# Kernel tuning notes

Measured on AMD Instinct MI355X. Metric: run time of the kernel, lower is better.

The kernel has to match this reference:

```python
import jax, jax.numpy as jnp
import numpy as np
import math

# ---- model dims (match init_kwargs) ----
D_MODEL = 1024
EXPAND = 2
HEADDIM = 64
D_STATE = 128
NGROUPS = 1
CHUNK = 64
A_FLOOR = 1e-4
D_INNER = EXPAND * D_MODEL            # 2048
NHEADS = D_INNER // HEADDIM           # 32
ROPE_DIM = D_STATE // 2               # rope_fraction=0.5 -> rotate half the state dims
NROPE = ROPE_DIM // 2                 # 32 rotation angles
D_IN_PROJ = D_INNER + 2 * D_STATE * NGROUPS + 3 * NHEADS + NROPE  # 2432
B, L = 2, 2048
EPS = 1e-5


def setup_inputs() -> dict:
    key = jax.random.key(0)
    ks = jax.random.split(key, 5)
    u = jax.random.normal(ks[0], (B, L, D_MODEL), dtype=jnp.float32)
    W_in = jax.random.normal(ks[1], (D_IN_PROJ, D_MODEL), dtype=jnp.float32) * 0.02
    W_out = jax.random.normal(ks[2], (D_MODEL, D_INNER), dtype=jnp.float32) * 0.02
    # dt_bias init as in the torch module
    dt_min, dt_max, dt_floor = 1e-3, 1e-1, 1e-4
    dt = jnp.exp(jax.random.uniform(ks[3], (NHEADS,)) * (math.log(dt_max) - math.log(dt_min)) + math.log(dt_min))
    dt = jnp.maximum(dt, dt_floor)
    dt_bias = dt + jnp.log(-jnp.expm1(-dt))
    B_bias = jnp.ones((NHEADS, D_STATE), dtype=jnp.float32)
    C_bias = jnp.ones((NHEADS, D_STATE), dtype=jnp.float32)
    Bnorm_w = jnp.ones((D_STATE,), dtype=jnp.float32)
    Cnorm_w = jnp.ones((D_STATE,), dtype=jnp.float32)
    D = jnp.ones((NHEADS,), dtype=jnp.float32)
    return {"u": u, "W_in": W_in, "dt_bias": dt_bias, "B_bias": B_bias, "C_bias": C_bias,
            "Bnorm_w": Bnorm_w, "Cnorm_w": Cnorm_w, "D": D, "W_out": W_out}


def _rmsnorm(v, w):
    return v * jax.lax.rsqrt(jnp.mean(v * v, axis=-1, keepdims=True) + EPS) * w


def _rope(v, cos, sin):
    # rotate first 2*NROPE dims of last axis (pairs (i, i+NROPE)); rest untouched
    x1 = v[..., :NROPE]
    x2 = v[..., NROPE:2 * NROPE]
    rest = v[..., 2 * NROPE:]
    return jnp.concatenate([x1 * cos - x2 * sin, x1 * sin + x2 * cos, rest], axis=-1)


def _forward(u, W_in, dt_bias, B_bias, C_bias, Bnorm_w, Cnorm_w, D, W_out):
    b, l, _ = u.shape
    proj = jnp.einsum('bld,ed->ble', u, W_in)
    idx = np.cumsum([D_INNER, D_STATE * NGROUPS, D_STATE * NGROUPS, NHEADS, NHEADS, NHEADS])[:-1].tolist()
    x, Braw, Craw, dd_dt, dd_A, trap_angles = jnp.split(proj, [D_INNER, D_INNER + D_STATE, D_INNER + 2 * D_STATE,
                                                                D_INNER + 2 * D_STATE + NHEADS,
                                                                D_INNER + 2 * D_STATE + 2 * NHEADS], axis=-1)
    trap = trap_angles[..., :NHEADS]
    angles = trap_angles[..., NHEADS:NHEADS + NROPE]
    x = x.reshape(b, l, NHEADS, HEADDIM)

    # discretization scalars per (b,l,h)
    A = -jax.nn.softplus(dd_A)
    A = jnp.minimum(A, -A_FLOOR)
    DT = jax.nn.softplus(dd_dt + dt_bias)
    la = A * DT                      # log of per-step decay (negative)
    a = jnp.exp(la)

    # RMSNorm on B/C (ngroups=1), broadcast to heads, add per-head bias
    Bn = _rmsnorm(Braw, Bnorm_w)[:, :, None, :] + B_bias   # (b,l,h,n)
    Cn = _rmsnorm(Craw, Cnorm_w)[:, :, None, :] + C_bias

    # inline RoPE: cumulative angle Theta_t = cumsum(angles_t * dt_t)
    theta = angles[:, :, None, :] * DT[..., None]           # (b,l,h,r)
    Theta = jnp.cumsum(theta, axis=1)
    cosT, sinT = jnp.cos(Theta), jnp.sin(Theta)
    Bn = _rope(Bn, cosT, sinT)
    Cn = _rope(Cn, cosT, sinT)

    # trapezoidal integration weights: dt*(lam*B_t x_t + (1-lam)*exp(A dt)*B_{t-1} x_{t-1})
    lam = jax.nn.sigmoid(trap)
    w1 = DT * lam                    # current-token weight  (b,l,h)
    w2 = DT * (1.0 - lam) * a        # previous-token weight (includes decay)
    Bp = jnp.pad(Bn, ((0, 0), (1, 0), (0, 0), (0, 0)))[:, :-1]
    xp = jnp.pad(x, ((0, 0), (1, 0), (0, 0), (0, 0)))[:, :-1]

    # ---- chunked selective scan ----
    nc = l // CHUNK
    ck = lambda t: t.reshape(b, nc, CHUNK, *t.shape[2:])
    xc, xpc, Bc, Bpc, Cc = ck(x), ck(xp), ck(Bn), ck(Bp), ck(Cn)
    lac, w1c, w2c = ck(la), ck(w1), ck(w2)
    Acum = jnp.cumsum(lac, axis=2)                           # (b,z,t,h)

    mask = jnp.tril(jnp.ones((CHUNK, CHUNK), dtype=u.dtype))
    decay = jnp.exp(Acum[:, :, :, None, :] - Acum[:, :, None, :, :]) * mask[None, None, :, :, None]  # (b,z,t,s,h)

    CB1 = jnp.einsum('bzthn,bzshn->bztsh', Cc, Bc)
    CB2 = jnp.einsum('bzthn,bzshn->bztsh', Cc, Bpc)
    M1 = decay * CB1 * w1c[:, :, None, :, :]
    M2 = decay * CB2 * w2c[:, :, None, :, :]
    Yintra = jnp.einsum('bztsh,bzshp->bzthp', M1, xc) + jnp.einsum('bztsh,bzshp->bzthp', M2, xpc)

    # contribution of each chunk to its end-of-chunk state
    r = jnp.exp(Acum[:, :, -1:, :] - Acum)                   # (b,z,t,h)
    U = (jnp.einsum('bzsh,bzshn,bzshp->bzhpn', r * w1c, Bc, xc)
         + jnp.einsum('bzsh,bzshn,bzshp->bzhpn', r * w2c, Bpc, xpc))
    cd = jnp.exp(Acum[:, :, -1, :])                          # whole-chunk decay (b,z,h)

    def step(h, inp):
        U_, c_ = inp
        return c_[..., None, None] * h + U_, h               # emit state at chunk start
    h0 = jnp.zeros((b, NHEADS, HEADDIM, D_STATE), dtype=u.dtype)
    _, states = jax.lax.scan(step, h0, (jnp.moveaxis(U, 1, 0), jnp.moveaxis(cd, 1, 0)))  # (z,b,h,p,n)

    Ystate = jnp.einsum('bzthn,bzth,zbhpn->bzthp', Cc, jnp.exp(Acum), states)
    y = (Yintra + Ystate).reshape(b, l, NHEADS, HEADDIM) + x * D[None, None, :, None]
    y = y.reshape(b, l, D_INNER)
    return jnp.einsum('bli,oi->blo', y, W_out)


def reference(u, W_in, dt_bias, B_bias, C_bias, Bnorm_w, Cnorm_w, D, W_out):
    return _forward(u, W_in, dt_bias, B_bias, C_bias, Bnorm_w, Cnorm_w, D, W_out)
```

## Files before the change

kernel.cpp:

```cpp
#include <hip/hip_runtime.h>
#include <hip/hip_bf16.h>
#include <math.h>

typedef unsigned short u16;
typedef __attribute__((ext_vector_type(8))) short s16x8;
typedef __attribute__((ext_vector_type(4))) float f32x4;

#define BB 2
#define LL 2048
#define DMODEL 1024
#define DI 2048
#define NH 32
#define HD 64
#define DS 128
#define NR 32
#define CH 64
#define NC 32
#define DIP 2432
#define NTOK (BB*LL)
#define PAW 384
#define CVW 264

__device__ __forceinline__ float bf2f(u16 u){ union{unsigned i; float f;} c; c.i=((unsigned)u)<<16; return c.f; }
__device__ __forceinline__ u16 f2bf(float f){ __hip_bfloat16 h=__float2bfloat16(f); return *reinterpret_cast<u16*>(&h); }
__device__ __forceinline__ float softplusf(float x){ return fmaxf(x,0.f) + log1pf(expf(-fabsf(x))); }

__device__ __forceinline__ void gl_lds16(const void* g, void* l){
  __builtin_amdgcn_global_load_lds((const __attribute__((address_space(1))) void*)g,
                                   (__attribute__((address_space(3))) void*)l, 16, 0, 0);
}

__device__ __forceinline__ s16x8 ldswz(const u16* base, int r, int kunit){
  return *(const s16x8*)&base[r*128 + ((kunit ^ (r&7))<<3)];
}
__device__ __forceinline__ s16x8 ldswz64(const u16* base, int r, int kunit){
  return *(const s16x8*)&base[r*64 + ((kunit ^ (r&7))<<3)];
}
__device__ __forceinline__ float ldswz64_s(const u16* base, int r, int n){
  return bf2f(base[r*64 + (((n>>3) ^ (r&7))<<3) + (n&7)]);
}
__device__ __forceinline__ s16x8 ld72(const u16* base, int r, int kelem){
  return *(const s16x8*)&base[r*72 + kelem];
}

__global__ __launch_bounds__(256) void k_cast(const float* __restrict__ in, u16* __restrict__ out, int n){
  int i = (blockIdx.x*256 + threadIdx.x)*4;
  if (i < n){
    float4 v = *(const float4*)&in[i];
    ushort4 o; o.x=f2bf(v.x); o.y=f2bf(v.y); o.z=f2bf(v.z); o.w=f2bf(v.w);
    *(ushort4*)&out[i] = o;
  }
}

__global__ __launch_bounds__(512) void k_gemm_in(const u16* __restrict__ A,
                                                 const u16* __restrict__ Bm,
                                                 float* __restrict__ pAux,
                                                 u16* __restrict__ Xtg){
  __shared__ u16 lA[128*64];
  __shared__ u16 lB[128*64];
  int tid = threadIdx.x;
  int l = tid & 63, w = tid >> 6;
  int nwg = gridDim.x*gridDim.y;
  int flat = blockIdx.y*gridDim.x + blockIdx.x;
  int cpx = nwg >> 3;
  int swz = (flat & 7)*cpx + (flat >> 3);
  int bx = swz % gridDim.x, by = swz / gridDim.x;
  int bm = by*128, bn = bx*128;
  int wr = w >> 2, wc = w & 3;
  const f32x4 vzero = {0.f,0.f,0.f,0.f};
  f32x4 acc[4][2];
  #pragma unroll
  for (int i=0;i<4;i++)
    #pragma unroll
    for (int j=0;j<2;j++) acc[i][j] = vzero;

  for (int kt=0; kt<DMODEL; kt+=64){
    __syncthreads();
    #pragma unroll
    for (int cc=0; cc<2; cc++){
      int s = w*2 + cc;
      int uu = s*64 + l;
      int r = uu >> 3, jl = uu & 7;
      int j = jl ^ (r & 7);
      gl_lds16(A  + (size_t)(bm+r)*DMODEL + kt + j*8, &lA[s*512]);
      gl_lds16(Bm + (size_t)(bn+r)*DMODEL + kt + j*8, &lB[s*512]);
    }
    __syncthreads();
    #pragma unroll
    for (int ks=0; ks<2; ks++){
      s16x8 af[4], bf[2];
      #pragma unroll
      for (int i=0;i<4;i++){
        int row = wr*64 + i*16 + (l&15);
        int j = ks*4 + (l>>4);
        af[i] = *(const s16x8*)&lA[row*64 + (j^(row&7))*8];
      }
      #pragma unroll
      for (int i=0;i<2;i++){
        int row = wc*32 + i*16 + (l&15);
        int j = ks*4 + (l>>4);
        bf[i] = *(const s16x8*)&lB[row*64 + (j^(row&7))*8];
      }
      #pragma unroll
      for (int i=0;i<4;i++)
        #pragma unroll
        for (int jj=0;jj<2;jj++)
          acc[i][jj] = __builtin_amdgcn_mfma_f32_16x16x32_bf16(af[i], bf[jj], acc[i][jj], 0,0,0);
    }
  }
  int col0 = bn + wc*32 + (l&15);
  int row0 = bm + wr*64 + (l>>4)*4;
  if (bn < DI){
    int h = (bn + wc*32) >> 6;
    int pbase = (wc & 1)*32 + (l&15);
    int b = bm >> 11;
    #pragma unroll
    for (int i=0;i<4;i++){
      int lbase = (bm & (LL-1)) + wr*64 + (l>>4)*4 + i*16;
      #pragma unroll
      for (int jj=0;jj<2;jj++){
        int p = pbase + jj*16;
        ushort4 o;
        o.x = f2bf(acc[i][jj][0]); o.y = f2bf(acc[i][jj][1]);
        o.z = f2bf(acc[i][jj][2]); o.w = f2bf(acc[i][jj][3]);
        *(ushort4*)&Xtg[((size_t)(b*NH + h)*HD + p)*LL + lbase] = o;
      }
    }
  } else {
    #pragma unroll
    for (int i=0;i<4;i++)
      #pragma unroll
      for (int jj=0;jj<2;jj++)
        #pragma unroll
        for (int q=0;q<4;q++)
          pAux[(size_t)(row0 + i*16 + q)*PAW + col0 + jj*16 - DI] = acc[i][jj][q];
  }
}

__global__ __launch_bounds__(256) void k_prep(const float* __restrict__ pAux,
                                              const float* __restrict__ dt_bias,
                                              const float* __restrict__ Bnw,
                                              const float* __restrict__ Cnw,
                                              float* __restrict__ Bnr, float* __restrict__ Cnr,
                                              float* __restrict__ DTg, float* __restrict__ lag,
                                              float* __restrict__ w1g, float* __restrict__ w2g){
  int tid = threadIdx.x;
  int r = tid >> 7, t = tid & 127;
  int row = blockIdx.x*2 + r;
  const float* pr = pAux + (size_t)row*PAW;
  float bv = pr[t], cv = pr[128+t];
  float sb = bv*bv, sc = cv*cv;
  for (int o=32;o;o>>=1){ sb += __shfl_down(sb,o); sc += __shfl_down(sc,o); }
  __shared__ float red[8];
  if ((tid&63)==0){ red[(tid>>6)*2]=sb; red[(tid>>6)*2+1]=sc; }
  __syncthreads();
  float ssb = red[r*4]+red[r*4+2], ssc = red[r*4+1]+red[r*4+3];
  float rb = rsqrtf(ssb/DS + 1e-5f), rc = rsqrtf(ssc/DS + 1e-5f);
  Bnr[(size_t)row*DS+t] = bv*rb*Bnw[t];
  Cnr[(size_t)row*DS+t] = cv*rc*Cnw[t];
  if (t < NH){
    int h = t;
    float Av = -softplusf(pr[288+h]); Av = fminf(Av, -1e-4f);
    float DT = softplusf(pr[256+h] + dt_bias[h]);
    float la = Av*DT;
    float lam = 1.f/(1.f+expf(-pr[320+h]));
    DTg[row*NH+h] = DT;
    lag[row*NH+h] = la;
    w1g[row*NH+h] = DT*lam;
    w2g[row*NH+h] = DT*(1.f-lam)*expf(la);
  }
}

__global__ __launch_bounds__(64) void k_theta_part(const float* __restrict__ pAux, const float* __restrict__ DTg,
                                                   float* __restrict__ Spart){
  int blk = blockIdx.x*2 + (threadIdx.x>>5);
  int j = threadIdx.x & 31;
  int h = blk % NH; int z = (blk/NH)%NC; int b = blk/(NH*NC);
  float acc = 0.f;
  for (int i=0;i<CH;i++){
    int row = b*LL + z*CH + i;
    acc += DTg[row*NH+h] * pAux[(size_t)row*PAW + 352 + j];
  }
  Spart[(size_t)blk*NR + j] = acc;
}

__global__ void k_theta_scan(float* __restrict__ Spart){
  int idx = blockIdx.x*blockDim.x + threadIdx.x;
  int j = idx % NR; int h = (idx/NR)%NH; int b = idx/(NR*NH);
  float acc = 0.f;
  for (int z=0;z<NC;z++){
    size_t o = (size_t)((b*NC+z)*NH + h)*NR + j;
    float t = Spart[o]; Spart[o] = acc; acc += t;
  }
}

__global__ __launch_bounds__(64) void k_theta_full(const float* __restrict__ pAux, const float* __restrict__ DTg,
                                                   const float* __restrict__ Spart, float* __restrict__ Theta){
  int blk = blockIdx.x*2 + (threadIdx.x>>5);
  int j = threadIdx.x & 31;
  int h = blk % NH; int z = (blk/NH)%NC; int b = blk/(NH*NC);
  float acc = Spart[(size_t)blk*NR + j];
  for (int i=0;i<CH;i++){
    int row = b*LL + z*CH + i;
    acc += DTg[row*NH+h] * pAux[(size_t)row*PAW + 352 + j];
    Theta[((size_t)row*NH + h)*NR + j] = acc;
  }
}

__global__ __launch_bounds__(256) void k_acum(const float* __restrict__ lag,
                                              const float* __restrict__ w1g,
                                              const float* __restrict__ w2g,
                                              float* __restrict__ CV,
                                              float* __restrict__ Acumg,
                                              float* __restrict__ cdg){
  int blk = blockIdx.x*4 + (threadIdx.x>>6);
  int l = threadIdx.x & 63;
  int h = blk & 31, z = (blk>>5)&31, b = blk>>10;
  int row = b*LL + z*CH + l;
  float la = lag[row*NH+h], w1 = w1g[row*NH+h], w2 = w2g[row*NH+h];
  float a = la;
  #pragma unroll
  for (int o=1;o<64;o<<=1){ float t = __shfl_up(a,o); a += (l>=o) ? t : 0.f; }
  float Acm = __shfl(a, 31);
  float Alast = __shfl(a, 63);
  float eA = expf(a - Acm);
  float emA = expf(Acm - a);
  float rfac = expf(Alast - a);
  float rw1 = rfac*w1, rw2 = rfac*w2;
  float rw1p = __shfl_up(rw1, 1);
  float* cv = CV + (size_t)blk*CVW;
  cv[l] = eA;
  cv[64 + l] = emA*w1;
  cv[128 + l] = emA*w2;
  cv[192 + l] = (l>0 ? rw1p : 0.f) + rw2;
  if (l == 63){ cv[192+64] = rw1; cdg[blk] = expf(Alast); }
  Acumg[(size_t)blk*CH + l] = a;
}

__global__ __launch_bounds__(256) void k_rope2(const float* __restrict__ Bnr,
                                               const float* __restrict__ Cnr,
                                               const float* __restrict__ Theta,
                                               const float* __restrict__ B_bias,
                                               const float* __restrict__ C_bias,
                                               const float* __restrict__ CV,
                                               u16* __restrict__ Bn, u16* __restrict__ Cn,
                                               u16* __restrict__ BTw){
  __shared__ float vwS[65];
  __shared__ u16 BTt[128][68];
  int blk = blockIdx.x; int h = blk&31, z=(blk>>5)&31, b=blk>>10;
  int l0 = z*CH; int tid = threadIdx.x;
  if (tid < 65) vwS[tid] = CV[(size_t)blk*CVW + 192 + tid];
  __syncthreads();
  #pragma unroll
  for (int it=0; it<8; it++){
    int idx = it*256 + tid;
    int r = idx>>5, j = idx&31;
    int row = b*LL + l0 + r;
    const float* br = Bnr + (size_t)row*DS;
    const float* cr = Cnr + (size_t)row*DS;
    const float* bb = B_bias + h*DS;
    const float* cb = C_bias + h*DS;
    float th = Theta[((size_t)row*NH + h)*NR + j];
    float cs = cosf(th), sn = sinf(th);
    float b0 = br[j]    + bb[j];
    float b1 = br[j+32] + bb[j+32];
    float b2 = br[j+64] + bb[j+64];
    float b3 = br[j+96] + bb[j+96];
    float c0 = cr[j]    + cb[j];
    float c1 = cr[j+32] + cb[j+32];
    float c2 = cr[j+64] + cb[j+64];
    float c3 = cr[j+96] + cb[j+96];
    float obA = b0*cs - b1*sn, obB = b0*sn + b1*cs;
    float ocA = c0*cs - c1*sn, ocB = c0*sn + c1*cs;
    u16* bnp = Bn + ((size_t)row*NH + h)*DS;
    u16* cnp = Cn + ((size_t)row*NH + h)*DS;
    bnp[j]    = f2bf(obA); bnp[j+32] = f2bf(obB);
    bnp[j+64] = f2bf(b2);  bnp[j+96] = f2bf(b3);
    cnp[j]    = f2bf(ocA); cnp[j+32] = f2bf(ocB);
    cnp[j+64] = f2bf(c2);  cnp[j+96] = f2bf(c3);
    float vwr = vwS[r+1];
    BTt[j][r]    = f2bf(obA*vwr);
    BTt[j+32][r] = f2bf(obB*vwr);
    BTt[j+64][r] = f2bf(b2*vwr);
    BTt[j+96][r] = f2bf(b3*vwr);
  }
  __syncthreads();
  for (int it=0; it<8; it++){
    int idx = it*256 + tid;
    int n = idx>>4, rg = (idx&15)*4;
    ushort4 o4;
    o4.x = BTt[n][rg];
    o4.y = BTt[n][rg+1];
    o4.z = BTt[n][rg+2];
    o4.w = BTt[n][rg+3];
    *(ushort4*)&BTw[((size_t)((b*NH+h)*DS) + n)*LL + l0 + rg] = o4;
  }
}

__global__ __launch_bounds__(256) void k_chunk_a(
    const u16* __restrict__ Xtg, const u16* __restrict__ Bn,
    const u16* __restrict__ Cn, const u16* __restrict__ BTw,
    const float* __restrict__ CV, const float* __restrict__ Dgl,
    u16* __restrict__ Yb, u16* __restrict__ Ugb){
  __shared__ u16 BsBT[65*128];
  __shared__ u16 CsMc[64*128];
  __shared__ u16 Xt64[64*64];
  __shared__ u16 Bp[128], Xp[64];
  __shared__ float cvS[260];
  __shared__ float mc0s[64];
  int blk = blockIdx.x;
  int h = blk&31, z=(blk>>5)&31, b=blk>>10;
  int l0 = z*CH;
  int tid = threadIdx.x; int l = tid&63, w = tid>>6;
  size_t bh = (size_t)(b*NH + h);

  if (tid < 128){
    u16 v = 0;
    if (z > 0) v = Bn[((size_t)(b*LL+l0-1)*NH + h)*DS + tid];
    BsBT[tid] = v; Bp[tid] = v;
  } else if (tid < 192){
    int p = tid - 128;
    u16 v = 0;
    if (z > 0) v = Xtg[(bh*HD + p)*LL + l0 - 1];
    Xp[p] = v;
  }
  cvS[tid] = CV[(size_t)blk*CVW + tid];
  if (tid == 0) cvS[256] = CV[(size_t)blk*CVW + 256];
  #pragma unroll
  for (int cc=0; cc<4; cc++){
    int c = w*4 + cc;
    { int r = 1 + 4*c + (l>>4);
      gl_lds16(Bn + ((size_t)(b*LL+l0+r-1)*NH+h)*DS + (((l&15)^(r&7))<<3), &BsBT[(1+4*c)*128]); }
    { int r = 4*c + (l>>4);
      gl_lds16(Cn + ((size_t)(b*LL+l0+r)*NH+h)*DS + (((l&15)^(r&7))<<3), &CsMc[4*c*128]); }
  }
  #pragma unroll
  for (int cc=0; cc<2; cc++){
    int s = w*2 + cc;
    int uu = s*64 + l; int r = uu>>3, jl = uu&7, j = jl^(r&7);
    gl_lds16(Xtg + (bh*HD + r)*LL + l0 + j*8, &Xt64[s*512]);
  }
  __syncthreads();

  const f32x4 vzero = {0.f,0.f,0.f,0.f};
  f32x4 acb[4];
  #pragma unroll
  for (int j=0;j<4;j++) acb[j] = vzero;
  #pragma unroll
  for (int ks=0; ks<4; ks++){
    s16x8 af = ldswz(CsMc, 16*w + (l&15), ks*4 + (l>>4));
    #pragma unroll
    for (int j=0;j<4;j++){
      s16x8 bfr = ldswz(BsBT, 1 + 16*j + (l&15), ks*4 + (l>>4));
      acb[j] = __builtin_amdgcn_mfma_f32_16x16x32_bf16(af, bfr, acb[j], 0,0,0);
    }
  }
  {
    int t = tid>>2, part = tid&3;
    float s = 0.f;
    #pragma unroll
    for (int uu=0; uu<4; uu++){
      int u = part*4 + uu;
      s16x8 cr = *(const s16x8*)&CsMc[t*128 + ((u^(t&7))<<3)];
      s16x8 br = *(const s16x8*)&BsBT[u<<3];
      #pragma unroll
      for (int e=0;e<8;e++) s += bf2f(cr[e])*bf2f(br[e]);
    }
    s += __shfl_xor(s, 1); s += __shfl_xor(s, 2);
    if (part == 0) mc0s[t] = s * cvS[t] * cvS[128];
  }
  __syncthreads();

  #pragma unroll
  for (int cc=0; cc<4; cc++){
    int c = w*4 + cc;
    int uu = c*64 + l; int r = uu>>3, jl = uu&7, j = jl^(r&7);
    gl_lds16(BTw + (bh*DS + r)*LL + l0 + j*8, &BsBT[c*512]);
  }
  #pragma unroll
  for (int j=0;j<4;j++){
    #pragma unroll
    for (int q=0;q<4;q++){
      int t = 16*w + (l>>4)*4 + q;
      int k = 16*j + (l&15);
      int sp = k + 1;
      float g = 0.f;
      if (sp <= t+1) g += cvS[63+sp];
      if (sp <= t)   g += cvS[128+sp];
      g *= cvS[t];
      CsMc[t*72 + k] = f2bf(acb[j][q] * g);
    }
  }
  __syncthreads();

  f32x4 ay[4];
  #pragma unroll
  for (int j=0;j<4;j++) ay[j] = vzero;
  #pragma unroll
  for (int ks=0; ks<2; ks++){
    s16x8 af = ld72(CsMc, 16*w + (l&15), ks*32 + (l>>4)*8);
    #pragma unroll
    for (int j=0;j<4;j++){
      s16x8 bfr = ldswz64(Xt64, 16*j + (l&15), ks*4 + (l>>4));
      ay[j] = __builtin_amdgcn_mfma_f32_16x16x32_bf16(af, bfr, ay[j], 0,0,0);
    }
  }
  {
    float Dh = Dgl[h];
    #pragma unroll
    for (int j=0;j<4;j++){
      #pragma unroll
      for (int q=0;q<4;q++){
        int t = 16*w + (l>>4)*4 + q;
        int p = 16*j + (l&15);
        float xval = ldswz64_s(Xt64, p, t);
        float yv = ay[j][q] + mc0s[t]*bf2f(Xp[p]) + Dh*xval;
        Yb[((size_t)(b*LL + l0 + t))*DI + h*HD + p] = f2bf(yv);
      }
    }
  }

  f32x4 au[8];
  #pragma unroll
  for (int j=0;j<8;j++) au[j] = vzero;
  #pragma unroll
  for (int ks=0; ks<2; ks++){
    s16x8 af = ldswz64(Xt64, 16*w + (l&15), ks*4 + (l>>4));
    #pragma unroll
    for (int j=0;j<8;j++){
      s16x8 bfr = ldswz64(BsBT, 16*j + (l&15), ks*4 + (l>>4));
      au[j] = __builtin_amdgcn_mfma_f32_16x16x32_bf16(af, bfr, au[j], 0,0,0);
    }
  }
  {
    float vw0 = cvS[192];
    #pragma unroll
    for (int j=0;j<8;j++){
      #pragma unroll
      for (int q=0;q<4;q++){
        int p = 16*w + (l>>4)*4 + q;
        int n = 16*j + (l&15);
        float uv = au[j][q] + vw0*bf2f(Xp[p])*bf2f(Bp[n]);
        Ugb[(size_t)blk*(HD*DS) + p*DS + n] = f2bf(uv);
      }
    }
  }
}

__global__ __launch_bounds__(256) void k_scan(u16* __restrict__ Ugb, const float* __restrict__ cdg){
  int idx = blockIdx.x*256 + threadIdx.x;
  int pn8 = (idx & 1023)*8;
  int h  = (idx >> 10) & 31;
  int b  = idx >> 15;
  float hs[8];
  #pragma unroll
  for (int e=0;e<8;e++) hs[e] = 0.f;
  for (int z=0;z<NC;z++){
    size_t o = ((size_t)((b*NC+z)*NH) + h)*(HD*DS) + pn8;
    s16x8 v = *(s16x8*)&Ugb[o];
    float cd = cdg[(b*NC+z)*NH + h];
    s16x8 wv;
    #pragma unroll
    for (int e=0;e<8;e++){
      float tmp = bf2f((u16)v[e]);
      wv[e] = (short)f2bf(hs[e]);
      hs[e] = cd*hs[e] + tmp;
    }
    *(s16x8*)&Ugb[o] = wv;
  }
}

__global__ __launch_bounds__(256) void k_state(
    const u16* __restrict__ Cn, const u16* __restrict__ Ugb,
    const float* __restrict__ Acumg, u16* __restrict__ Yb){
  __shared__ u16 Cs[64*128];
  __shared__ u16 Sb[64*128];
  __shared__ float eAs[64];
  int blk = blockIdx.x;
  int h = blk & 31, z = (blk>>5)&31, b = blk>>10;
  int l0 = z*CH;
  int tid = threadIdx.x;
  int l = tid & 63, w = tid >> 6;

  if (tid < 64) eAs[tid] = expf(Acumg[(size_t)blk*CH + tid]);
  #pragma unroll
  for (int cc=0; cc<4; cc++){
    int c = w*4 + cc;
    int r = 4*c + (l>>4);
    gl_lds16(Cn + ((size_t)(b*LL + l0 + r)*NH + h)*DS + (((l&15)^(r&7))<<3), &Cs[4*c*128]);
    gl_lds16(Ugb + (size_t)blk*(HD*DS) + (size_t)r*DS + (((l&15)^(r&7))<<3), &Sb[4*c*128]);
  }
  __syncthreads();

  f32x4 as[4];
  const f32x4 vzero = {0.f,0.f,0.f,0.f};
  #pragma unroll
  for (int j=0;j<4;j++) as[j] = vzero;
  #pragma unroll
  for (int ks=0; ks<4; ks++){
    s16x8 af = ldswz(Cs, 16*w + (l&15), ks*4 + (l>>4));
    #pragma unroll
    for (int j=0;j<4;j++){
      s16x8 bfr = ldswz(Sb, 16*j + (l&15), ks*4 + (l>>4));
      as[j] = __builtin_amdgcn_mfma_f32_16x16x32_bf16(af, bfr, as[j], 0,0,0);
    }
  }
  #pragma unroll
  for (int j=0;j<4;j++){
    #pragma unroll
    for (int q=0;q<4;q++){
      int t = 16*w + (l>>4)*4 + q;
      int p = 16*j + (l&15);
      size_t idx = ((size_t)(b*LL + l0 + t))*DI + h*HD + p;
      Yb[idx] = f2bf(bf2f(Yb[idx]) + eAs[t]*as[j][q]);
    }
  }
}

template<int N, int K>
__global__ __launch_bounds__(512) void k_mfma_nt(const u16* __restrict__ A,
                                                 const u16* __restrict__ Bm,
                                                 float* __restrict__ C){
  __shared__ u16 lA[128*64];
  __shared__ u16 lB[128*64];
  int tid = threadIdx.x;
  int l = tid & 63, w = tid >> 6;
  int nwg = gridDim.x*gridDim.y;
  int flat = blockIdx.y*gridDim.x + blockIdx.x;
  int cpx = nwg >> 3;
  int swz = (flat & 7)*cpx + (flat >> 3);
  int bx = swz % gridDim.x, by = swz / gridDim.x;
  int bm = by*128, bn = bx*128;
  int wr = w >> 2, wc = w & 3;
  const f32x4 vzero = {0.f,0.f,0.f,0.f};
  f32x4 acc[4][2];
  #pragma unroll
  for (int i=0;i<4;i++)
    #pragma unroll
    for (int j=0;j<2;j++) acc[i][j] = vzero;

  for (int kt=0; kt<K; kt+=64){
    __syncthreads();
    #pragma unroll
    for (int cc=0; cc<2; cc++){
      int s = w*2 + cc;
      int uu = s*64 + l;
      int r = uu >> 3, jl = uu & 7;
      int j = jl ^ (r & 7);
      gl_lds16(A  + (size_t)(bm+r)*K + kt + j*8, &lA[s*512]);
      gl_lds16(Bm + (size_t)(bn+r)*K + kt + j*8, &lB[s*512]);
    }
    __syncthreads();
    #pragma unroll
    for (int ks=0; ks<2; ks++){
      s16x8 af[4], bf[2];
      #pragma unroll
      for (int i=0;i<4;i++){
        int row = wr*64 + i*16 + (l&15);
        int j = ks*4 + (l>>4);
        af[i] = *(const s16x8*)&lA[row*64 + (j^(row&7))*8];
      }
      #pragma unroll
      for (int i=0;i<2;i++){
        int row = wc*32 + i*16 + (l&15);
        int j = ks*4 + (l>>4);
        bf[i] = *(const s16x8*)&lB[row*64 + (j^(row&7))*8];
      }
      #pragma unroll
      for (int i=0;i<4;i++)
        #pragma unroll
        for (int jj=0;jj<2;jj++)
          acc[i][jj] = __builtin_amdgcn_mfma_f32_16x16x32_bf16(af[i], bf[jj], acc[i][jj], 0,0,0);
    }
  }
  int col0 = bn + wc*32 + (l&15);
  int row0 = bm + wr*64 + (l>>4)*4;
  #pragma unroll
  for (int i=0;i<4;i++)
    #pragma unroll
    for (int jj=0;jj<2;jj++)
      #pragma unroll
      for (int q=0;q<4;q++)
        C[(size_t)(row0 + i*16 + q)*N + col0 + jj*16] = acc[i][jj][q];
}

constexpr size_t OFF_PAUX  = 0;
constexpr size_t OFF_XTG   = 6291456;
constexpr size_t OFF_BNR   = 23068672;
constexpr size_t OFF_CNR   = 25165824;
constexpr size_t OFF_DT    = 27262976;
constexpr size_t OFF_LA    = 27787264;
constexpr size_t OFF_W1    = 28311552;
constexpr size_t OFF_W2    = 28835840;
constexpr size_t OFF_SPART = 29360128;
constexpr size_t OFF_CV    = 29622272;
constexpr size_t OFF_ACUM  = 31784960;
constexpr size_t OFF_CD    = 32309248;
constexpr size_t OFF_THETA = 32317440;
constexpr size_t OFF_Y     = OFF_THETA;
constexpr size_t OFF_BN    = 49094656;
constexpr size_t OFF_CN    = 82649088;
constexpr size_t OFF_BTW   = 116203520;
constexpr size_t OFF_R1    = 149757952;
constexpr size_t OFF_UBF   = OFF_R1;
constexpr size_t OFF_WINBF = OFF_R1 + 16777216;
constexpr size_t OFF_UGB   = OFF_R1;
constexpr size_t OFF_WOUTBF= OFF_PAUX;

extern "C" void kernel_launch(void* const* d_in, const int* in_sizes, int n_in,
                              void* d_out, int out_size, void* d_ws, size_t ws_size,
                              hipStream_t stream) {
  const float* u       = (const float*)d_in[0];
  const float* W_in    = (const float*)d_in[1];
  const float* dt_bias = (const float*)d_in[2];
  const float* B_bias  = (const float*)d_in[3];
  const float* C_bias  = (const float*)d_in[4];
  const float* Bnw     = (const float*)d_in[5];
  const float* Cnw     = (const float*)d_in[6];
  const float* Dg      = (const float*)d_in[7];
  const float* W_out   = (const float*)d_in[8];
  float* out = (float*)d_out;
  char* ws = (char*)d_ws;

  float* pAux  = (float*)(ws + OFF_PAUX);
  u16*   Xtg   = (u16*)  (ws + OFF_XTG);
  float* Bnr   = (float*)(ws + OFF_BNR);
  float* Cnr   = (float*)(ws + OFF_CNR);
  float* DTg   = (float*)(ws + OFF_DT);
  float* lag   = (float*)(ws + OFF_LA);
  float* w1g   = (float*)(ws + OFF_W1);
  float* w2g   = (float*)(ws + OFF_W2);
  float* Spart = (float*)(ws + OFF_SPART);
  float* CVp   = (float*)(ws + OFF_CV);
  float* Acumg = (float*)(ws + OFF_ACUM);
  float* cdg   = (float*)(ws + OFF_CD);
  float* Theta = (float*)(ws + OFF_THETA);
  u16*   Yb    = (u16*)  (ws + OFF_Y);
  u16*   Bn    = (u16*)  (ws + OFF_BN);
  u16*   Cn    = (u16*)  (ws + OFF_CN);
  u16*   BTw   = (u16*)  (ws + OFF_BTW);
  u16*   u_bf  = (u16*)  (ws + OFF_UBF);
  u16*   Win_bf= (u16*)  (ws + OFF_WINBF);
  u16*   Ugb   = (u16*)  (ws + OFF_UGB);
  u16*   Wout_bf=(u16*)  (ws + OFF_WOUTBF);

  k_cast<<<(NTOK*DMODEL)/1024, 256, 0, stream>>>(u, u_bf, NTOK*DMODEL);
  k_cast<<<(DIP*DMODEL)/1024, 256, 0, stream>>>(W_in, Win_bf, DIP*DMODEL);
  k_gemm_in<<<dim3(DIP/128, NTOK/128), 512, 0, stream>>>(u_bf, Win_bf, pAux, Xtg);

  k_prep      <<<NTOK/2, 256, 0, stream>>>(pAux, dt_bias, Bnw, Cnw, Bnr, Cnr, DTg, lag, w1g, w2g);
  k_theta_part<<<(BB*NC*NH)/2, 64, 0, stream>>>(pAux, DTg, Spart);
  k_theta_scan<<<(BB*NH*NR)/256, 256, 0, stream>>>(Spart);
  k_theta_full<<<(BB*NC*NH)/2, 64, 0, stream>>>(pAux, DTg, Spart, Theta);
  k_acum      <<<(BB*NC*NH)/4, 256, 0, stream>>>(lag, w1g, w2g, CVp, Acumg, cdg);
  k_rope2     <<<BB*NC*NH, 256, 0, stream>>>(Bnr, Cnr, Theta, B_bias, C_bias, CVp, Bn, Cn, BTw);

  k_chunk_a<<<BB*NC*NH, 256, 0, stream>>>(Xtg, Bn, Cn, BTw, CVp, Dg, Yb, Ugb);
  k_scan   <<<(BB*NH*HD*DS)/(256*8), 256, 0, stream>>>(Ugb, cdg);
  k_state  <<<BB*NC*NH, 256, 0, stream>>>(Cn, Ugb, Acumg, Yb);

  k_cast<<<(DMODEL*DI)/1024, 256, 0, stream>>>(W_out, Wout_bf, DMODEL*DI);
  k_mfma_nt<DMODEL, DI><<<dim3(DMODEL/128, NTOK/128), 512, 0, stream>>>(Yb, Wout_bf, out);

  (void)in_sizes; (void)n_in; (void)out_size; (void)ws_size;
}
```

Measured before the change: 190.8 us.

## Merge three cast kernels and double waves per block in chunk and state kernels

The three fp32-to-bf16 casts (u, W_in, W_out) now run as one launch, and the W_out buffer moves to its own workspace offset so it can be converted up front. k_chunk_a and k_state go from 256 to 512 threads, with the 8 waves split into a 4x2 grid over the MFMA output tiles, so each wave holds fewer accumulators and issues fewer MFMAs. This cuts launch overhead and raises per-block parallelism, but adds a branch to the cast kernel and larger blocks that may lower occupancy.

```diff
diff --git a/kernel.cpp b/kernel.cpp
--- a/kernel.cpp
+++ b/kernel.cpp
@@ -43,13 +43,22 @@
   return *(const s16x8*)&base[r*72 + kelem];
 }
 
-__global__ __launch_bounds__(256) void k_cast(const float* __restrict__ in, u16* __restrict__ out, int n){
-  int i = (blockIdx.x*256 + threadIdx.x)*4;
-  if (i < n){
-    float4 v = *(const float4*)&in[i];
-    ushort4 o; o.x=f2bf(v.x); o.y=f2bf(v.y); o.z=f2bf(v.z); o.w=f2bf(v.w);
-    *(ushort4*)&out[i] = o;
-  }
+#define CQ1 ((NTOK*DMODEL)/4)
+#define CQ2 ((DIP*DMODEL)/4)
+#define CQ3 ((DMODEL*DI)/4)
+__global__ __launch_bounds__(256) void k_cast3(const float* __restrict__ u, const float* __restrict__ Wi,
+                                               const float* __restrict__ Wo,
+                                               u16* __restrict__ ub, u16* __restrict__ wib,
+                                               u16* __restrict__ wob){
+  int i = blockIdx.x*256 + threadIdx.x;
+  const float* src; u16* dst; int q;
+  if (i < CQ1){ src = u; dst = ub; q = i; }
+  else if (i < CQ1+CQ2){ src = Wi; dst = wib; q = i - CQ1; }
+  else if (i < CQ1+CQ2+CQ3){ src = Wo; dst = wob; q = i - CQ1 - CQ2; }
+  else return;
+  float4 v = *(const float4*)&src[(size_t)q*4];
+  ushort4 o; o.x=f2bf(v.x); o.y=f2bf(v.y); o.z=f2bf(v.z); o.w=f2bf(v.w);
+  *(ushort4*)&dst[(size_t)q*4] = o;
 }
 
 __global__ __launch_bounds__(512) void k_gemm_in(const u16* __restrict__ A,
@@ -297,7 +306,7 @@
   }
 }
 
-__global__ __launch_bounds__(256) void k_chunk_a(
+__global__ __launch_bounds__(512) void k_chunk_a(
     const u16* __restrict__ Xtg, const u16* __restrict__ Bn,
     const u16* __restrict__ Cn, const u16* __restrict__ BTw,
     const float* __restrict__ CV, const float* __restrict__ Dgl,
@@ -312,6 +321,7 @@
   int h = blk&31, z=(blk>>5)&31, b=blk>>10;
   int l0 = z*CH;
   int tid = threadIdx.x; int l = tid&63, w = tid>>6;
+  int wA = w >> 1, wB = w & 1;
   size_t bh = (size_t)(b*NH + h);
 
   if (tid < 128){
@@ -324,65 +334,62 @@
     if (z > 0) v = Xtg[(bh*HD + p)*LL + l0 - 1];
     Xp[p] = v;
   }
-  cvS[tid] = CV[(size_t)blk*CVW + tid];
-  if (tid == 0) cvS[256] = CV[(size_t)blk*CVW + 256];
-  #pragma unroll
-  for (int cc=0; cc<4; cc++){
-    int c = w*4 + cc;
+  if (tid < 257) cvS[tid] = CV[(size_t)blk*CVW + tid];
+  #pragma unroll
+  for (int cc=0; cc<2; cc++){
+    int c = w*2 + cc;
     { int r = 1 + 4*c + (l>>4);
       gl_lds16(Bn + ((size_t)(b*LL+l0+r-1)*NH+h)*DS + (((l&15)^(r&7))<<3), &BsBT[(1+4*c)*128]); }
     { int r = 4*c + (l>>4);
       gl_lds16(Cn + ((size_t)(b*LL+l0+r)*NH+h)*DS + (((l&15)^(r&7))<<3), &CsMc[4*c*128]); }
   }
-  #pragma unroll
-  for (int cc=0; cc<2; cc++){
-    int s = w*2 + cc;
-    int uu = s*64 + l; int r = uu>>3, jl = uu&7, j = jl^(r&7);
-    gl_lds16(Xtg + (bh*HD + r)*LL + l0 + j*8, &Xt64[s*512]);
+  {
+    int uu = w*64 + l; int r = uu>>3, jl = uu&7, j = jl^(r&7);
+    gl_lds16(Xtg + (bh*HD + r)*LL + l0 + j*8, &Xt64[w*512]);
   }
   __syncthreads();
 
   const f32x4 vzero = {0.f,0.f,0.f,0.f};
-  f32x4 acb[4];
-  #pragma unroll
-  for (int j=0;j<4;j++) acb[j] = vzero;
+  f32x4 acb[2];
+  #pragma unroll
+  for (int j=0;j<2;j++) acb[j] = vzero;
   #pragma unroll
   for (int ks=0; ks<4; ks++){
-    s16x8 af = ldswz(CsMc, 16*w + (l&15), ks*4 + (l>>4));
-    #pragma unroll
-    for (int j=0;j<4;j++){
-      s16x8 bfr = ldswz(BsBT, 1 + 16*j + (l&15), ks*4 + (l>>4));
+    s16x8 af = ldswz(CsMc, 16*wA + (l&15), ks*4 + (l>>4));
+    #pragma unroll
+    for (int j=0;j<2;j++){
+      s16x8 bfr = ldswz(BsBT, 1 + 16*(wB*2+j) + (l&15), ks*4 + (l>>4));
       acb[j] = __builtin_amdgcn_mfma_f32_16x16x32_bf16(af, bfr, acb[j], 0,0,0);
     }
   }
   {
-    int t = tid>>2, part = tid&3;
+    int t = tid>>3, part = tid&7;
     float s = 0.f;
     #pragma unroll
-    for (int uu=0; uu<4; uu++){
-      int u = part*4 + uu;
+    for (int uu=0; uu<2; uu++){
+      int u = part*2 + uu;
       s16x8 cr = *(const s16x8*)&CsMc[t*128 + ((u^(t&7))<<3)];
       s16x8 br = *(const s16x8*)&BsBT[u<<3];
       #pragma unroll
       for (int e=0;e<8;e++) s += bf2f(cr[e])*bf2f(br[e]);
     }
-    s += __shfl_xor(s, 1); s += __shfl_xor(s, 2);
+    s += __shfl_xor(s, 1); s += __shfl_xor(s, 2); s += __shfl_xor(s, 4);
     if (part == 0) mc0s[t] = s * cvS[t] * cvS[128];
   }
   __syncthreads();
 
   #pragma unroll
-  for (int cc=0; cc<4; cc++){
-    int c = w*4 + cc;
+  for (int cc=0; cc<2; cc++){
+    int c = w*2 + cc;
     int uu = c*64 + l; int r = uu>>3, jl = uu&7, j = jl^(r&7);
     gl_lds16(BTw + (bh*DS + r)*LL + l0 + j*8, &BsBT[c*512]);
   }
   #pragma unroll
-  for (int j=0;j<4;j++){
+  for (int j=0;j<2;j++){
     #pragma unroll
     for (int q=0;q<4;q++){
-      int t = 16*w + (l>>4)*4 + q;
-      int k = 16*j + (l&15);
+      int t = 16*wA + (l>>4)*4 + q;
+      int k = 16*(wB*2+j) + (l&15);
       int sp = k + 1;
       float g = 0.f;
       if (sp <= t+1) g += cvS[63+sp];
@@ -393,26 +400,26 @@
   }
   __syncthreads();
 
-  f32x4 ay[4];
-  #pragma unroll
-  for (int j=0;j<4;j++) ay[j] = vzero;
+  f32x4 ay[2];
+  #pragma unroll
+  for (int j=0;j<2;j++) ay[j] = vzero;
   #pragma unroll
   for (int ks=0; ks<2; ks++){
-    s16x8 af = ld72(CsMc, 16*w + (l&15), ks*32 + (l>>4)*8);
-    #pragma unroll
-    for (int j=0;j<4;j++){
-      s16x8 bfr = ldswz64(Xt64, 16*j + (l&15), ks*4 + (l>>4));
+    s16x8 af = ld72(CsMc, 16*wA + (l&15), ks*32 + (l>>4)*8);
+    #pragma unroll
+    for (int j=0;j<2;j++){
+      s16x8 bfr = ldswz64(Xt64, 16*(wB*2+j) + (l&15), ks*4 + (l>>4));
       ay[j] = __builtin_amdgcn_mfma_f32_16x16x32_bf16(af, bfr, ay[j], 0,0,0);
     }
   }
   {
     float Dh = Dgl[h];
     #pragma unroll
-    for (int j=0;j<4;j++){
+    for (int j=0;j<2;j++){
       #pragma unroll
       for (int q=0;q<4;q++){
-        int t = 16*w + (l>>4)*4 + q;
-        int p = 16*j + (l&15);
+        int t = 16*wA + (l>>4)*4 + q;
+        int p = 16*(wB*2+j) + (l&15);
         float xval = ldswz64_s(Xt64, p, t);
         float yv = ay[j][q] + mc0s[t]*bf2f(Xp[p]) + Dh*xval;
         Yb[((size_t)(b*LL + l0 + t))*DI + h*HD + p] = f2bf(yv);
@@ -420,26 +427,26 @@
     }
   }
 
-  f32x4 au[8];
-  #pragma unroll
-  for (int j=0;j<8;j++) au[j] = vzero;
+  f32x4 au[4];
+  #pragma unroll
+  for (int j=0;j<4;j++) au[j] = vzero;
   #pragma unroll
   for (int ks=0; ks<2; ks++){
-    s16x8 af = ldswz64(Xt64, 16*w + (l&15), ks*4 + (l>>4));
-    #pragma unroll
-    for (int j=0;j<8;j++){
-      s16x8 bfr = ldswz64(BsBT, 16*j + (l&15), ks*4 + (l>>4));
+    s16x8 af = ldswz64(Xt64, 16*wA + (l&15), ks*4 + (l>>4));
+    #pragma unroll
+    for (int j=0;j<4;j++){
+      s16x8 bfr = ldswz64(BsBT, 16*(wB*4+j) + (l&15), ks*4 + (l>>4));
       au[j] = __builtin_amdgcn_mfma_f32_16x16x32_bf16(af, bfr, au[j], 0,0,0);
     }
   }
   {
     float vw0 = cvS[192];
     #pragma unroll
-    for (int j=0;j<8;j++){
+    for (int j=0;j<4;j++){
       #pragma unroll
       for (int q=0;q<4;q++){
-        int p = 16*w + (l>>4)*4 + q;
-        int n = 16*j + (l&15);
+        int p = 16*wA + (l>>4)*4 + q;
+        int n = 16*(wB*4+j) + (l&15);
         float uv = au[j][q] + vw0*bf2f(Xp[p])*bf2f(Bp[n]);
         Ugb[(size_t)blk*(HD*DS) + p*DS + n] = f2bf(uv);
       }
@@ -470,7 +477,7 @@
   }
 }
 
-__global__ __launch_bounds__(256) void k_state(
+__global__ __launch_bounds__(512) void k_state(
     const u16* __restrict__ Cn, const u16* __restrict__ Ugb,
     const float* __restrict__ Acumg, u16* __restrict__ Yb){
   __shared__ u16 Cs[64*128];
@@ -481,36 +488,37 @@
   int l0 = z*CH;
   int tid = threadIdx.x;
   int l = tid & 63, w = tid >> 6;
+  int wA = w >> 1, wB = w & 1;
 
   if (tid < 64) eAs[tid] = expf(Acumg[(size_t)blk*CH + tid]);
   #pragma unroll
-  for (int cc=0; cc<4; cc++){
-    int c = w*4 + cc;
+  for (int cc=0; cc<2; cc++){
+    int c = w*2 + cc;
     int r = 4*c + (l>>4);
     gl_lds16(Cn + ((size_t)(b*LL + l0 + r)*NH + h)*DS + (((l&15)^(r&7))<<3), &Cs[4*c*128]);
     gl_lds16(Ugb + (size_t)blk*(HD*DS) + (size_t)r*DS + (((l&15)^(r&7))<<3), &Sb[4*c*128]);
   }
   __syncthreads();
 
-  f32x4 as[4];
+  f32x4 as[2];
   const f32x4 vzero = {0.f,0.f,0.f,0.f};
   #pragma unroll
-  for (int j=0;j<4;j++) as[j] = vzero;
+  for (int j=0;j<2;j++) as[j] = vzero;
   #pragma unroll
   for (int ks=0; ks<4; ks++){
-    s16x8 af = ldswz(Cs, 16*w + (l&15), ks*4 + (l>>4));
-    #pragma unroll
-    for (int j=0;j<4;j++){
-      s16x8 bfr = ldswz(Sb, 16*j + (l&15), ks*4 + (l>>4));
+    s16x8 af = ldswz(Cs, 16*wA + (l&15), ks*4 + (l>>4));
+    #pragma unroll
+    for (int j=0;j<2;j++){
+      s16x8 bfr = ldswz(Sb, 16*(wB*2+j) + (l&15), ks*4 + (l>>4));
       as[j] = __builtin_amdgcn_mfma_f32_16x16x32_bf16(af, bfr, as[j], 0,0,0);
     }
   }
   #pragma unroll
-  for (int j=0;j<4;j++){
+  for (int j=0;j<2;j++){
     #pragma unroll
     for (int q=0;q<4;q++){
-      int t = 16*w + (l>>4)*4 + q;
-      int p = 16*j + (l&15);
+      int t = 16*wA + (l>>4)*4 + q;
+      int p = 16*(wB*2+j) + (l&15);
       size_t idx = ((size_t)(b*LL + l0 + t))*DI + h*HD + p;
       Yb[idx] = f2bf(bf2f(Yb[idx]) + eAs[t]*as[j][q]);
     }
@@ -605,7 +613,7 @@
 constexpr size_t OFF_UBF   = OFF_R1;
 constexpr size_t OFF_WINBF = OFF_R1 + 16777216;
 constexpr size_t OFF_UGB   = OFF_R1;
-constexpr size_t OFF_WOUTBF= OFF_PAUX;
+constexpr size_t OFF_WOUTBF= 183312384;
 
 extern "C" void kernel_launch(void* const* d_in, const int* in_sizes, int n_in,
                               void* d_out, int out_size, void* d_ws, size_t ws_size,
@@ -644,8 +652,7 @@
   u16*   Ugb   = (u16*)  (ws + OFF_UGB);
   u16*   Wout_bf=(u16*)  (ws + OFF_WOUTBF);
 
-  k_cast<<<(NTOK*DMODEL)/1024, 256, 0, stream>>>(u, u_bf, NTOK*DMODEL);
-  k_cast<<<(DIP*DMODEL)/1024, 256, 0, stream>>>(W_in, Win_bf, DIP*DMODEL);
+  k_cast3<<<(CQ1+CQ2+CQ3+255)/256, 256, 0, stream>>>(u, W_in, W_out, u_bf, Win_bf, Wout_bf);
   k_gemm_in<<<dim3(DIP/128, NTOK/128), 512, 0, stream>>>(u_bf, Win_bf, pAux, Xtg);
 
   k_prep      <<<NTOK/2, 256, 0, stream>>>(pAux, dt_bias, Bnw, Cnw, Bnr, Cnr, DTg, lag, w1g, w2g);
@@ -655,11 +662,10 @@
   k_acum      <<<(BB*NC*NH)/4, 256, 0, stream>>>(lag, w1g, w2g, CVp, Acumg, cdg);
   k_rope2     <<<BB*NC*NH, 256, 0, stream>>>(Bnr, Cnr, Theta, B_bias, C_bias, CVp, Bn, Cn, BTw);
 
-  k_chunk_a<<<BB*NC*NH, 256, 0, stream>>>(Xtg, Bn, Cn, BTw, CVp, Dg, Yb, Ugb);
+  k_chunk_a<<<BB*NC*NH, 512, 0, stream>>>(Xtg, Bn, Cn, BTw, CVp, Dg, Yb, Ugb);
   k_scan   <<<(BB*NH*HD*DS)/(256*8), 256, 0, stream>>>(Ugb, cdg);
-  k_state  <<<BB*NC*NH, 256, 0, stream>>>(Cn, Ugb, Acumg, Yb);
-
-  k_cast<<<(DMODEL*DI)/1024, 256, 0, stream>>>(W_out, Wout_bf, DMODEL*DI);
+  k_state  <<<BB*NC*NH, 512, 0, stream>>>(Cn, Ugb, Acumg, Yb);
+
   k_mfma_nt<DMODEL, DI><<<dim3(DMODEL/128, NTOK/128), 512, 0, stream>>>(Yb, Wout_bf, out);
 
   (void)in_sizes; (void)n_in; (void)out_size; (void)ws_size;
```

After: 182.8 us. -4.2%, faster.
